# Kernel tuning notes

Measured on AMD Instinct MI355X. Metric: run time of the kernel, lower is better.

The kernel has to match this reference:

```python
import jax, jax.numpy as jnp
import numpy as np

H = 1024
V = 5000
NUM_LAYERS = 2
B, T, U = 2, 128, 64


def setup_inputs() -> dict:
    key = jax.random.key(0)
    ks = jax.random.split(key, 16)
    s = 0.02
    inp = {
        "encoder_out": jax.random.normal(ks[0], (B, T, H), dtype=jnp.float32),
        "targets": jax.random.randint(ks[1], (B, U), 0, V),
        "embed": jax.random.normal(ks[2], (V, H), dtype=jnp.float32) * s,
        # stacked 2-layer LSTM params, PyTorch gate order (i, f, g, o)
        "lstm_Wih": jax.random.normal(ks[3], (NUM_LAYERS, 4 * H, H), dtype=jnp.float32) * s,
        "lstm_Whh": jax.random.normal(ks[4], (NUM_LAYERS, 4 * H, H), dtype=jnp.float32) * s,
        "lstm_bih": jnp.zeros((NUM_LAYERS, 4 * H), dtype=jnp.float32),
        "lstm_bhh": jnp.zeros((NUM_LAYERS, 4 * H), dtype=jnp.float32),
        "enc_W": jax.random.normal(ks[5], (H, H), dtype=jnp.float32) * s,
        "enc_b": jnp.zeros((H,), dtype=jnp.float32),
        "pred_W": jax.random.normal(ks[6], (H, H), dtype=jnp.float32) * s,
        "pred_b": jnp.zeros((H,), dtype=jnp.float32),
        "out_W": jax.random.normal(ks[7], (V + 1, H), dtype=jnp.float32) * s,
        "out_b": jnp.zeros((V + 1,), dtype=jnp.float32),
    }
    return inp


def _lstm_layer(x, Wih, Whh, bih, bhh):
    # x: [B, U, H] -> [B, U, H]; single LSTM layer, PyTorch gate order i,f,g,o
    b, u, h = x.shape
    bias = bih + bhh  # [4H]
    # precompute input projections for all timesteps: [U, B, 4H]
    xg = jnp.einsum('buh,gh->ubg', x, Wih) + bias

    def step(carry, xt):
        hprev, cprev = carry
        gates = xt + hprev @ Whh.T  # [B, 4H]
        i, f, g, o = jnp.split(gates, 4, axis=-1)
        i = jax.nn.sigmoid(i)
        f = jax.nn.sigmoid(f)
        g = jnp.tanh(g)
        o = jax.nn.sigmoid(o)
        c = f * cprev + i * g
        hnew = o * jnp.tanh(c)
        return (hnew, c), hnew

    init = (jnp.zeros((b, h), x.dtype), jnp.zeros((b, h), x.dtype))
    _, hs = jax.lax.scan(step, init, xg)  # hs: [U, B, H]
    return hs.transpose(1, 0, 2)


def reference(encoder_out, targets, embed, lstm_Wih, lstm_Whh, lstm_bih, lstm_bhh,
              enc_W, enc_b, pred_W, pred_b, out_W, out_b):
    # Prediction network: embedding + 2-layer LSTM (deterministic -> no dropout)
    x = embed[targets]  # [B, U, H]
    for l in range(NUM_LAYERS):
        x = _lstm_layer(x, lstm_Wih[l], lstm_Whh[l], lstm_bih[l], lstm_bhh[l])
    pred_out = x  # [B, U, H]

    # Joint network: proj + broadcast add over (T, U) + ReLU + output linear
    enc_p = jnp.einsum('bth,oh->bto', encoder_out, enc_W) + enc_b  # [B, T, H]
    prd_p = jnp.einsum('buh,oh->buo', pred_out, pred_W) + pred_b    # [B, U, H]
    joint = jax.nn.relu(enc_p[:, :, None, :] + prd_p[:, None, :, :])  # [B, T, U, H]
    logits = jnp.einsum('btuh,vh->btuv', joint, out_W) + out_b  # [B, T, U, V+1]
    return logits
```

## Files before the change

kernel.cpp:

```cpp
#include <hip/hip_runtime.h>
#include <hip/hip_bf16.h>

#define B_ 2
#define T_ 128
#define U_ 64
#define H_ 1024
#define NO_ 5001

typedef __attribute__((ext_vector_type(8))) short bf16x8;
typedef __attribute__((ext_vector_type(4))) float f32x4;
typedef __attribute__((ext_vector_type(4))) unsigned int uint4v;

__device__ __forceinline__ float bf2f(unsigned short s) {
  unsigned int u = ((unsigned int)s) << 16;
  float f; __builtin_memcpy(&f, &u, 4); return f;
}
__device__ __forceinline__ unsigned short f2bf(float f) {
  unsigned int u; __builtin_memcpy(&u, &f, 4);
  u = u + 0x7FFFu + ((u >> 16) & 1u);
  return (unsigned short)(u >> 16);
}

__device__ __forceinline__ void gload_lds16(const unsigned short* g, unsigned short* l) {
  __builtin_amdgcn_global_load_lds(
      (const __attribute__((address_space(1))) unsigned int*)g,
      (__attribute__((address_space(3))) unsigned int*)l,
      16, 0, 0);
}

#define R_OUTW 1280256
#define R_WIH  (R_OUTW + 2097152)
#define R_WHH  (R_WIH + 2097152)
#define R_ENCW (R_WHH + 262144)
#define R_PRDW (R_ENCW + 262144)
#define R_ENC  (R_PRDW + 65536)
#define R_BIAS (R_ENC + 1280)

__global__ void k_cvt_all(
    const float* __restrict__ outW, const float* __restrict__ Wih,
    const float* __restrict__ Whh,  const float* __restrict__ encW,
    const float* __restrict__ prdW, const float* __restrict__ enc,
    const float* __restrict__ outB,
    unsigned short* __restrict__ outW_bf, unsigned short* __restrict__ Wih_bf,
    unsigned short* __restrict__ Whh_bf,  unsigned short* __restrict__ encW_bf,
    unsigned short* __restrict__ prdW_bf, unsigned short* __restrict__ enc_bf,
    float* __restrict__ biasPad)
{
  int i = blockIdx.x * 256 + threadIdx.x;
  const float* src; unsigned short* dst; int off;
  if (i < R_OUTW)      { src = outW; dst = outW_bf; off = i; }
  else if (i < R_WIH)  { src = Wih;  dst = Wih_bf;  off = i - R_OUTW; }
  else if (i < R_WHH)  { src = Whh;  dst = Whh_bf;  off = i - R_WIH; }
  else if (i < R_ENCW) { src = encW; dst = encW_bf; off = i - R_WHH; }
  else if (i < R_PRDW) { src = prdW; dst = prdW_bf; off = i - R_ENCW; }
  else if (i < R_ENC)  { src = enc;  dst = enc_bf;  off = i - R_PRDW; }
  else {
    int e0 = (i - R_ENC) * 4;
    float4 v;
    v.x = (e0 + 0 < NO_) ? outB[e0 + 0] : 0.f;
    v.y = (e0 + 1 < NO_) ? outB[e0 + 1] : 0.f;
    v.z = (e0 + 2 < NO_) ? outB[e0 + 2] : 0.f;
    v.w = (e0 + 3 < NO_) ? outB[e0 + 3] : 0.f;
    *(float4*)&biasPad[e0] = v;
    return;
  }
  const float4 v = ((const float4*)src)[off];
  ushort4 o;
  o.x = f2bf(v.x); o.y = f2bf(v.y); o.z = f2bf(v.z); o.w = f2bf(v.w);
  ((ushort4*)dst)[off] = o;
}

__global__ void k_embed(const int* __restrict__ tg, const float* __restrict__ em,
                        unsigned short* __restrict__ x0) {
  int idx = blockIdx.x * 256 + threadIdx.x;
  int bu = idx >> 8;
  int kc = (idx & 255) << 2;
  int t = tg[bu];
  const float4 v = *(const float4*)&em[(long)t * H_ + kc];
  ushort4 o; o.x = f2bf(v.x); o.y = f2bf(v.y); o.z = f2bf(v.z); o.w = f2bf(v.w);
  *(ushort4*)&x0[bu * H_ + kc] = o;
}

__global__ __launch_bounds__(256) void gemm_bt(
    const unsigned short* __restrict__ A, const unsigned short* __restrict__ W,
    const float* __restrict__ b1, const float* __restrict__ b2,
    float* __restrict__ C, int M, int N, int K)
{
  __shared__ unsigned short As[128 * 32];
  __shared__ unsigned short Bs[128 * 32];
  const int tid = threadIdx.x;
  const int n0 = blockIdx.x * 128, m0 = blockIdx.y * 128;
  const int lane = tid & 63, w = tid >> 6;
  const int wr = (w >> 1) * 64, wc = (w & 1) * 64;
  const int lr = lane & 15, lk = (lane >> 4) * 8;
  f32x4 acc[4][4] = {};

  for (int k0 = 0; k0 < K; k0 += 32) {
#pragma unroll
    for (int s = 0; s < 2; ++s) {
      int idx = (w * 2 + s) * 64 + lane;
      int row = idx >> 2, c8 = (idx & 3) * 8;
      gload_lds16(&A[(long)(m0 + row) * K + k0 + c8], &As[(w * 2 + s) * 512]);
      gload_lds16(&W[(long)(n0 + row) * K + k0 + c8], &Bs[(w * 2 + s) * 512]);
    }
    __syncthreads();
    bf16x8 aF[4], bF[4];
#pragma unroll
    for (int i = 0; i < 4; ++i) {
      aF[i] = *(const bf16x8*)&As[(wr + i * 16 + lr) * 32 + lk];
      bF[i] = *(const bf16x8*)&Bs[(wc + i * 16 + lr) * 32 + lk];
    }
#pragma unroll
    for (int i = 0; i < 4; ++i)
#pragma unroll
      for (int j = 0; j < 4; ++j)
        acc[i][j] = __builtin_amdgcn_mfma_f32_16x16x32_bf16(aF[i], bF[j], acc[i][j], 0, 0, 0);
    __syncthreads();
  }

  const int lq = (lane >> 4) * 4;
#pragma unroll
  for (int j = 0; j < 4; ++j) {
    int col = n0 + wc + j * 16 + lr;
    if (col >= N) continue;
    float bb = 0.f;
    if (b1) bb += b1[col];
    if (b2) bb += b2[col];
#pragma unroll
    for (int i = 0; i < 4; ++i) {
      int rowg = m0 + wr + i * 16 + lq;
#pragma unroll
      for (int r = 0; r < 4; ++r)
        C[(long)(rowg + r) * N + col] = acc[i][j][r] + bb;
    }
  }
}

#define STAGE_A(kt2, kh, rb) \
  gload_lds16(aSrc[rb] + (kt2) * 64 + (kh) * 32, \
              &As_f[((((kt2) & 1) * 2 + (kh)) * 8192) + ((rb) * 128 + wv * 16) * 32])
#define STAGE_B(kt2, kh, rb) \
  gload_lds16(bSrc[rb] + (kt2) * 64 + (kh) * 32, \
              &Bs_f[((((kt2) & 1) * 2 + (kh)) * 8192) + ((rb) * 128 + wv * 16) * 32])

__global__ __launch_bounds__(512, 1) void gemm_logits(
    const unsigned short* __restrict__ A, const unsigned short* __restrict__ W,
    const float* __restrict__ biasPad, float* __restrict__ C, int M, int N, int K)
{
  __shared__ __align__(16) unsigned short lds_all[65536];
  unsigned short* As_f = lds_all;
  unsigned short* Bs_f = lds_all + 32768;
  const int tid = threadIdx.x;
  const int lane = tid & 63, wv = tid >> 6;
  const int wm = wv >> 2, wn = wv & 3;
  int swzb = (blockIdx.x & 7) * 160 + (blockIdx.x >> 3);
  const int n0 = (swzb >> 6) * 256;
  const int m0 = (swzb & 63) * 256;
  const int NT = K / 64;

  const unsigned short* aSrc[2];
  const unsigned short* bSrc[2];
#pragma unroll
  for (int rb = 0; rb < 2; ++rb) {
    int rl = rb * 128 + (tid >> 2);
    int c2s = (tid & 3) ^ ((rl >> 1) & 3);
    aSrc[rb] = A + (long)(m0 + rl) * K + c2s * 8;
    bSrc[rb] = W + (long)(n0 + rl) * K + c2s * 8;
  }
  int aOff[8], bOff[4];
#pragma unroll
  for (int i = 0; i < 8; ++i) {
    int r = wm * 128 + i * 16 + (lane & 15);
    aOff[i] = r * 32 + (((lane >> 4) ^ ((r >> 1) & 3)) * 8);
  }
#pragma unroll
  for (int j = 0; j < 4; ++j) {
    int r = wn * 64 + j * 16 + (lane & 15);
    bOff[j] = r * 32 + (((lane >> 4) ^ ((r >> 1) & 3)) * 8);
  }

  f32x4 acc[8][4] = {};

  STAGE_A(0, 0, 0); STAGE_A(0, 0, 1); STAGE_B(0, 0, 0); STAGE_B(0, 0, 1);
  STAGE_A(0, 1, 0); STAGE_A(0, 1, 1); STAGE_B(0, 1, 0); STAGE_B(0, 1, 1);

  for (int kt = 0; kt < NT; ++kt) {
    const int b = kt & 1;
    asm volatile("s_waitcnt vmcnt(4)" ::: "memory");
    __builtin_amdgcn_s_barrier();
    __builtin_amdgcn_sched_barrier(0);
    {
      const int base = (b * 2 + 0) * 8192;
      bf16x8 aF[8], bF[4];
#pragma unroll
      for (int i = 0; i < 8; ++i) aF[i] = *(const bf16x8*)&As_f[base + aOff[i]];
#pragma unroll
      for (int j = 0; j < 4; ++j) bF[j] = *(const bf16x8*)&Bs_f[base + bOff[j]];
      if (kt + 1 < NT) {
        STAGE_A(kt + 1, 0, 0); STAGE_A(kt + 1, 0, 1);
        STAGE_B(kt + 1, 0, 0); STAGE_B(kt + 1, 0, 1);
        STAGE_A(kt + 1, 1, 0); STAGE_A(kt + 1, 1, 1);
      }
      __builtin_amdgcn_s_setprio(1);
#pragma unroll
      for (int i = 0; i < 8; ++i)
#pragma unroll
        for (int j = 0; j < 4; ++j)
          acc[i][j] = __builtin_amdgcn_mfma_f32_16x16x32_bf16(aF[i], bF[j], acc[i][j], 0, 0, 0);
      __builtin_amdgcn_s_setprio(0);
    }
    if (kt + 1 < NT) { asm volatile("s_waitcnt vmcnt(6)" ::: "memory"); }
    else             { asm volatile("s_waitcnt vmcnt(0)" ::: "memory"); }
    __builtin_amdgcn_s_barrier();
    __builtin_amdgcn_sched_barrier(0);
    {
      const int base = (b * 2 + 1) * 8192;
      bf16x8 aF[8], bF[4];
#pragma unroll
      for (int i = 0; i < 8; ++i) aF[i] = *(const bf16x8*)&As_f[base + aOff[i]];
#pragma unroll
      for (int j = 0; j < 4; ++j) bF[j] = *(const bf16x8*)&Bs_f[base + bOff[j]];
      if (kt + 1 < NT) { STAGE_B(kt + 1, 1, 0); STAGE_B(kt + 1, 1, 1); }
      __builtin_amdgcn_s_setprio(1);
#pragma unroll
      for (int i = 0; i < 8; ++i)
#pragma unroll
        for (int j = 0; j < 4; ++j)
          acc[i][j] = __builtin_amdgcn_mfma_f32_16x16x32_bf16(aF[i], bF[j], acc[i][j], 0, 0, 0);
      __builtin_amdgcn_s_setprio(0);
    }
  }

  float* eb = (float*)lds_all;
  const int lq = (lane >> 4) * 4;
  float bv4[4];
#pragma unroll
  for (int j = 0; j < 4; ++j) bv4[j] = biasPad[n0 + wn * 64 + j * 16 + (lane & 15)];

#pragma unroll
  for (int cp = 0; cp < 4; ++cp) {
    __syncthreads();
#pragma unroll
    for (int ii = 0; ii < 2; ++ii) {
      int rbase = wm * 32 + ii * 16 + lq;
#pragma unroll
      for (int j = 0; j < 4; ++j) {
        int col = wn * 64 + j * 16 + (lane & 15);
#pragma unroll
        for (int r = 0; r < 4; ++r)
          eb[(rbase + r) * 261 + col] = acc[cp * 2 + ii][j][r] + bv4[j];
      }
    }
    __syncthreads();
    {
      int rl = tid >> 3, ci = tid & 7;
      long grow = (long)m0 + (rl >> 5) * 128 + cp * 32 + (rl & 31);
      float* crow = C + grow * N + n0;
      const float* er = &eb[rl * 261];
#pragma unroll
      for (int k = 0; k < 8; ++k) {
        int col = ci * 4 + k * 32;
        float4 v = *(const float4*)&er[col];
        int gc = n0 + col;
        if (gc + 4 <= N) {
          *(float4*)&crow[col] = v;
        } else if (gc < N) {
          float tmp[4] = {v.x, v.y, v.z, v.w};
#pragma unroll
          for (int e = 0; e < 4; ++e)
            if (gc + e < N) crow[col + e] = tmp[e];
        }
      }
    }
  }
}

__global__ __launch_bounds__(256, 1) void lstm_fused3(
    const float* __restrict__ xg0,
    const unsigned short* __restrict__ Whh0,
    const unsigned short* __restrict__ Whh1,
    const unsigned short* __restrict__ Wih1,
    const float* __restrict__ bih1, const float* __restrict__ bhh1,
    unsigned short* __restrict__ x2_bf,
    float* __restrict__ hbuf0,
    float* __restrict__ hbuf1,
    float* __restrict__ xbuf,
    float* __restrict__ xgbuf,
    int*   __restrict__ flagsx)
{
  __shared__ float hs[2][H_];
  __shared__ float xgs[128][64];
  __shared__ float part[4][64][2];
  __shared__ float gv[2][64];
  __shared__ float bias2s[64];

  const int tid = threadIdx.x;
  const int grp = blockIdx.x >> 6;
  const int bid = blockIdx.x & 63;
  const int w = tid >> 6, l = tid & 63;
  const int g = l >> 4, q = l & 15;
  const int row = g * 1024 + bid * 16 + q;
  const int kb = w * 256;

  if (grp == 0) {
    bf16x8 wreg[32];
#pragma unroll
    for (int it = 0; it < 32; ++it)
      wreg[it] = *(const bf16x8*)&Whh0[(long)row * H_ + kb + it * 8];
#pragma unroll
    for (int rep = 0; rep < 8; ++rep) {
      int c = rep * 256 + tid;
      int r2 = c >> 4, sub = c & 15;
      int gg = sub >> 2, f4 = sub & 3;
      const float4 v = *(const float4*)&xg0[(long)r2 * 4096 + gg * 1024 + bid * 16 + f4 * 4];
      *(float4*)&xgs[r2][gg * 16 + f4 * 4] = v;
    }
    __syncthreads();

    float creg = 0.f;
    for (int u = 0; u < U_; ++u) {
      float a00 = 0.f, a01 = 0.f, a02 = 0.f, a03 = 0.f;
      float a10 = 0.f, a11 = 0.f, a12 = 0.f, a13 = 0.f;
      if (u > 0) {
        const float thr = 4.0f * u - 2.0f;
        const float* base = hbuf0 + (u & 1) * 2 * H_;
        const float* pa = base + tid * 4;
        const float* pb = base + H_ + tid * 4;
        float4 va, vb;
        for (;;) {
          asm volatile("global_load_dwordx4 %0, %2, off sc1\n\t"
                       "global_load_dwordx4 %1, %3, off sc1\n\t"
                       "s_waitcnt vmcnt(0)"
                       : "=v"(va), "=v"(vb) : "v"(pa), "v"(pb) : "memory");
          if (va.x > thr && va.y > thr && va.z > thr && va.w > thr &&
              vb.x > thr && vb.y > thr && vb.z > thr && vb.w > thr) break;
        }
        const float off = 4.0f * u;
        va.x -= off; va.y -= off; va.z -= off; va.w -= off;
        vb.x -= off; vb.y -= off; vb.z -= off; vb.w -= off;
        *(float4*)&hs[0][tid * 4] = va;
        *(float4*)&hs[1][tid * 4] = vb;
        __syncthreads();
#pragma unroll
        for (int it = 0; it < 32; ++it) {
          bf16x8 wv = wreg[it];
          float4 h0a = *(const float4*)&hs[0][kb + it * 8];
          float4 h0b = *(const float4*)&hs[0][kb + it * 8 + 4];
          float4 h1a = *(const float4*)&hs[1][kb + it * 8];
          float4 h1b = *(const float4*)&hs[1][kb + it * 8 + 4];
          a00 += bf2f((unsigned short)wv[0]) * h0a.x + bf2f((unsigned short)wv[4]) * h0b.x;
          a01 += bf2f((unsigned short)wv[1]) * h0a.y + bf2f((unsigned short)wv[5]) * h0b.y;
          a02 += bf2f((unsigned short)wv[2]) * h0a.z + bf2f((unsigned short)wv[6]) * h0b.z;
          a03 += bf2f((unsigned short)wv[3]) * h0a.w + bf2f((unsigned short)wv[7]) * h0b.w;
          a10 += bf2f((unsigned short)wv[0]) * h1a.x + bf2f((unsigned short)wv[4]) * h1b.x;
          a11 += bf2f((unsigned short)wv[1]) * h1a.y + bf2f((unsigned short)wv[5]) * h1b.y;
          a12 += bf2f((unsigned short)wv[2]) * h1a.z + bf2f((unsigned short)wv[6]) * h1b.z;
          a13 += bf2f((unsigned short)wv[3]) * h1a.w + bf2f((unsigned short)wv[7]) * h1b.w;
        }
      }
      part[w][l][0] = (a00 + a01) + (a02 + a03);
      part[w][l][1] = (a10 + a11) + (a12 + a13);
      __syncthreads();
      if (tid < 128) {
        int b = tid >> 6, ll = tid & 63;
        gv[b][ll] = part[0][ll][b] + part[1][ll][b] + part[2][ll][b] + part[3][ll][b]
                  + xgs[b * 64 + u][ll];
      }
      __syncthreads();
      if (tid < 32) {
        int b = tid >> 4, qq = tid & 15;
        float gi = gv[b][qq], gf = gv[b][16 + qq], gc = gv[b][32 + qq], go = gv[b][48 + qq];
        float i_ = 1.f / (1.f + expf(-gi));
        float f_ = 1.f / (1.f + expf(-gf));
        float g_ = tanhf(gc);
        float o_ = 1.f / (1.f + expf(-go));
        creg = f_ * creg + i_ * g_;
        float h = o_ * tanhf(creg);
        int j = bid * 16 + qq;
        float tvx = h + 4.0f;
        const float* px = &xbuf[u * 2 * H_ + b * H_ + j];
        asm volatile("global_store_dword %0, %1, off sc1" :: "v"(px), "v"(tvx) : "memory");
        if (u < U_ - 1) {
          float tv = h + 4.0f * (u + 1);
          const float* p = &hbuf0[((u + 1) & 1) * 2 * H_ + b * H_ + j];
          asm volatile("global_store_dword %0, %1, off sc1" :: "v"(p), "v"(tv) : "memory");
        }
      }
    }
  } else if (grp == 1) {
    bf16x8 wreg[32];
#pragma unroll
    for (int it = 0; it < 32; ++it)
      wreg[it] = *(const bf16x8*)&Wih1[(long)row * H_ + kb + it * 8];
    if (tid < 64) {
      int rr = (tid >> 4) * 1024 + bid * 16 + (tid & 15);
      bias2s[tid] = bih1[rr] + bhh1[rr];
    }
    __syncthreads();

    for (int u = 0; u < U_; ++u) {
      const float* base = xbuf + u * 2 * H_;
      const float* pa = base + tid * 4;
      const float* pb = base + H_ + tid * 4;
      float4 va, vb;
      for (;;) {
        asm volatile("global_load_dwordx4 %0, %2, off sc1\n\t"
                     "global_load_dwordx4 %1, %3, off sc1\n\t"
                     "s_waitcnt vmcnt(0)"
                     : "=v"(va), "=v"(vb) : "v"(pa), "v"(pb) : "memory");
        if (va.x > 2.f && va.y > 2.f && va.z > 2.f && va.w > 2.f &&
            vb.x > 2.f && vb.y > 2.f && vb.z > 2.f && vb.w > 2.f) break;
        __builtin_amdgcn_s_sleep(2);
      }
      va.x -= 4.f; va.y -= 4.f; va.z -= 4.f; va.w -= 4.f;
      vb.x -= 4.f; vb.y -= 4.f; vb.z -= 4.f; vb.w -= 4.f;
      *(float4*)&hs[0][tid * 4] = va;
      *(float4*)&hs[1][tid * 4] = vb;
      __syncthreads();

      float a00 = 0.f, a01 = 0.f, a02 = 0.f, a03 = 0.f;
      float a10 = 0.f, a11 = 0.f, a12 = 0.f, a13 = 0.f;
#pragma unroll
      for (int it = 0; it < 32; ++it) {
        bf16x8 wv = wreg[it];
        float4 h0a = *(const float4*)&hs[0][kb + it * 8];
        float4 h0b = *(const float4*)&hs[0][kb + it * 8 + 4];
        float4 h1a = *(const float4*)&hs[1][kb + it * 8];
        float4 h1b = *(const float4*)&hs[1][kb + it * 8 + 4];
        a00 += bf2f((unsigned short)wv[0]) * h0a.x + bf2f((unsigned short)wv[4]) * h0b.x;
        a01 += bf2f((unsigned short)wv[1]) * h0a.y + bf2f((unsigned short)wv[5]) * h0b.y;
        a02 += bf2f((unsigned short)wv[2]) * h0a.z + bf2f((unsigned short)wv[6]) * h0b.z;
        a03 += bf2f((unsigned short)wv[3]) * h0a.w + bf2f((unsigned short)wv[7]) * h0b.w;
        a10 += bf2f((unsigned short)wv[0]) * h1a.x + bf2f((unsigned short)wv[4]) * h1b.x;
        a11 += bf2f((unsigned short)wv[1]) * h1a.y + bf2f((unsigned short)wv[5]) * h1b.y;
        a12 += bf2f((unsigned short)wv[2]) * h1a.z + bf2f((unsigned short)wv[6]) * h1b.z;
        a13 += bf2f((unsigned short)wv[3]) * h1a.w + bf2f((unsigned short)wv[7]) * h1b.w;
      }
      part[w][l][0] = (a00 + a01) + (a02 + a03);
      part[w][l][1] = (a10 + a11) + (a12 + a13);
      __syncthreads();
      if (tid < 128) {
        int b = tid >> 6, ll = tid & 63;
        float s = part[0][ll][b] + part[1][ll][b] + part[2][ll][b] + part[3][ll][b]
                + bias2s[ll];
        const float* p = &xgbuf[((u * 64 + bid) * 2 + b) * 64 + ll];
        asm volatile("global_store_dword %0, %1, off sc1" :: "v"(p), "v"(s) : "memory");
        asm volatile("s_waitcnt vmcnt(0)" ::: "memory");
      }
      __syncthreads();
      if (tid == 0) {
        int one = 1;
        const int* fp = &flagsx[(u * 64 + bid) * 16];
        asm volatile("global_store_dword %0, %1, off sc1" :: "v"(fp), "v"(one) : "memory");
      }
    }
  } else {
    bf16x8 wreg[32];
#pragma unroll
    for (int it = 0; it < 32; ++it)
      wreg[it] = *(const bf16x8*)&Whh1[(long)row * H_ + kb + it * 8];
    __syncthreads();

    float creg = 0.f;
    for (int u = 0; u < U_; ++u) {
      {
        const int* fp = &flagsx[(u * 64 + bid) * 16];
        int fv;
        do {
          asm volatile("global_load_dword %0, %1, off sc1\n\ts_waitcnt vmcnt(0)"
                       : "=v"(fv) : "v"(fp) : "memory");
        } while (fv == 0);
      }
      float xgv = 0.f;
      if (tid < 128) {
        const float* p = &xgbuf[((u * 64 + bid) * 2 + (tid >> 6)) * 64 + (tid & 63)];
        asm volatile("global_load_dword %0, %1, off sc1\n\ts_waitcnt vmcnt(0)"
                     : "=v"(xgv) : "v"(p) : "memory");
      }
      float a00 = 0.f, a01 = 0.f, a02 = 0.f, a03 = 0.f;
      float a10 = 0.f, a11 = 0.f, a12 = 0.f, a13 = 0.f;
      if (u > 0) {
        const float thr = 4.0f * u - 2.0f;
        const float* base = hbuf1 + (u & 1) * 2 * H_;
        const float* pa = base + tid * 4;
        const float* pb = base + H_ + tid * 4;
        float4 va, vb;
        for (;;) {
          asm volatile("global_load_dwordx4 %0, %2, off sc1\n\t"
                       "global_load_dwordx4 %1, %3, off sc1\n\t"
                       "s_waitcnt vmcnt(0)"
                       : "=v"(va), "=v"(vb) : "v"(pa), "v"(pb) : "memory");
          if (va.x > thr && va.y > thr && va.z > thr && va.w > thr &&
              vb.x > thr && vb.y > thr && vb.z > thr && vb.w > thr) break;
        }
        const float off = 4.0f * u;
        va.x -= off; va.y -= off; va.z -= off; va.w -= off;
        vb.x -= off; vb.y -= off; vb.z -= off; vb.w -= off;
        *(float4*)&hs[0][tid * 4] = va;
        *(float4*)&hs[1][tid * 4] = vb;
        __syncthreads();
#pragma unroll
        for (int it = 0; it < 32; ++it) {
          bf16x8 wv = wreg[it];
          float4 h0a = *(const float4*)&hs[0][kb + it * 8];
          float4 h0b = *(const float4*)&hs[0][kb + it * 8 + 4];
          float4 h1a = *(const float4*)&hs[1][kb + it * 8];
          float4 h1b = *(const float4*)&hs[1][kb + it * 8 + 4];
          a00 += bf2f((unsigned short)wv[0]) * h0a.x + bf2f((unsigned short)wv[4]) * h0b.x;
          a01 += bf2f((unsigned short)wv[1]) * h0a.y + bf2f((unsigned short)wv[5]) * h0b.y;
          a02 += bf2f((unsigned short)wv[2]) * h0a.z + bf2f((unsigned short)wv[6]) * h0b.z;
          a03 += bf2f((unsigned short)wv[3]) * h0a.w + bf2f((unsigned short)wv[7]) * h0b.w;
          a10 += bf2f((unsigned short)wv[0]) * h1a.x + bf2f((unsigned short)wv[4]) * h1b.x;
          a11 += bf2f((unsigned short)wv[1]) * h1a.y + bf2f((unsigned short)wv[5]) * h1b.y;
          a12 += bf2f((unsigned short)wv[2]) * h1a.z + bf2f((unsigned short)wv[6]) * h1b.z;
          a13 += bf2f((unsigned short)wv[3]) * h1a.w + bf2f((unsigned short)wv[7]) * h1b.w;
        }
      }
      part[w][l][0] = (a00 + a01) + (a02 + a03);
      part[w][l][1] = (a10 + a11) + (a12 + a13);
      __syncthreads();
      if (tid < 128) {
        int b = tid >> 6, ll = tid & 63;
        gv[b][ll] = part[0][ll][b] + part[1][ll][b] + part[2][ll][b] + part[3][ll][b]
                  + xgv;
      }
      __syncthreads();
      if (tid < 32) {
        int b = tid >> 4, qq = tid & 15;
        float gi = gv[b][qq], gf = gv[b][16 + qq], gc = gv[b][32 + qq], go = gv[b][48 + qq];
        float i_ = 1.f / (1.f + expf(-gi));
        float f_ = 1.f / (1.f + expf(-gf));
        float g_ = tanhf(gc);
        float o_ = 1.f / (1.f + expf(-go));
        creg = f_ * creg + i_ * g_;
        float h = o_ * tanhf(creg);
        int j = bid * 16 + qq;
        x2_bf[(b * U_ + u) * H_ + j] = f2bf(h);
        if (u < U_ - 1) {
          float tv = h + 4.0f * (u + 1);
          const float* p = &hbuf1[((u + 1) & 1) * 2 * H_ + b * H_ + j];
          asm volatile("global_store_dword %0, %1, off sc1" :: "v"(p), "v"(tv) : "memory");
        }
      }
    }
  }
}

__global__ void k_joint(const float* __restrict__ ep, const float* __restrict__ pp,
                        unsigned short* __restrict__ jt)
{
  int idx = blockIdx.x * 256 + threadIdx.x;
  int m = idx >> 8;
  int kc = (idx & 255) << 2;
  int erow = m >> 6;
  int prow = (m >> 13) * U_ + (m & 63);
  const float4 e = *(const float4*)&ep[erow * H_ + kc];
  const float4 p = *(const float4*)&pp[prow * H_ + kc];
  float4 s;
  s.x = fmaxf(e.x + p.x, 0.f); s.y = fmaxf(e.y + p.y, 0.f);
  s.z = fmaxf(e.z + p.z, 0.f); s.w = fmaxf(e.w + p.w, 0.f);
  ushort4 o; o.x = f2bf(s.x); o.y = f2bf(s.y); o.z = f2bf(s.z); o.w = f2bf(s.w);
  *(ushort4*)&jt[m * H_ + kc] = o;
}

extern "C" void kernel_launch(void* const* d_in, const int* in_sizes, int n_in,
                              void* d_out, int out_size, void* d_ws, size_t ws_size,
                              hipStream_t stream)
{
  const float* enc   = (const float*)d_in[0];
  const int*   tg    = (const int*)d_in[1];
  const float* em    = (const float*)d_in[2];
  const float* Wih   = (const float*)d_in[3];
  const float* Whh   = (const float*)d_in[4];
  const float* bih   = (const float*)d_in[5];
  const float* bhh   = (const float*)d_in[6];
  const float* encW  = (const float*)d_in[7];
  const float* encB  = (const float*)d_in[8];
  const float* prdW  = (const float*)d_in[9];
  const float* prdB  = (const float*)d_in[10];
  const float* outW  = (const float*)d_in[11];
  const float* outB  = (const float*)d_in[12];
  float* out = (float*)d_out;
  char* ws = (char*)d_ws;

  unsigned short* outW_bf = (unsigned short*)(ws + 0);
  unsigned short* Wih_bf  = (unsigned short*)(ws + 10485760);
  unsigned short* Whh_bf  = (unsigned short*)(ws + 27262976);
  unsigned short* encW_bf = (unsigned short*)(ws + 44040192);
  unsigned short* prdW_bf = (unsigned short*)(ws + 46137344);
  unsigned short* enc_bf  = (unsigned short*)(ws + 48234496);
  unsigned short* x0_bf   = (unsigned short*)(ws + 48758784);
  unsigned short* x2_bf   = (unsigned short*)(ws + 49283072);
  float* xg  = (float*)(ws + 49545216);
  float* hbufL0 = (float*)(ws + 51642368);
  unsigned short* jt = (unsigned short*)(ws + 51659008);
  float* hbufL1 = (float*)(ws + 85213440);
  float* biasPad = (float*)(ws + 85229824);
  float* xbuf = (float*)(ws + 85250304);
  int* flagsx = (int*)(ws + 85774592);
  float* xgbuf = xg;
  float* ep = xg;
  float* pp = (float*)(ws + 49545216 + 1048576);

  hipMemsetAsync(hbufL0, 0, 16384, stream);
  hipMemsetAsync(hbufL1, 0, 16384, stream);
  hipMemsetAsync(xbuf, 0, 524288, stream);
  hipMemsetAsync(flagsx, 0, 262144, stream);

  k_cvt_all<<<R_BIAS / 256, 256, 0, stream>>>(
      outW, Wih, Whh, encW, prdW, enc, outB,
      outW_bf, Wih_bf, Whh_bf, encW_bf, prdW_bf, enc_bf, biasPad);
  k_embed<<<(B_ * U_ * H_ / 4) / 256, 256, 0, stream>>>(tg, em, x0_bf);

  gemm_bt<<<dim3(32, 1), 256, 0, stream>>>(x0_bf, Wih_bf, bih, bhh, xg, B_ * U_, 4096, H_);
  lstm_fused3<<<192, 256, 0, stream>>>(xg, Whh_bf, Whh_bf + 4096 * H_, Wih_bf + 4096 * H_,
                                       bih + 4096, bhh + 4096, x2_bf,
                                       hbufL0, hbufL1, xbuf, xgbuf, flagsx);

  gemm_bt<<<dim3(8, 2), 256, 0, stream>>>(enc_bf, encW_bf, encB, nullptr, ep, B_ * T_, H_, H_);
  gemm_bt<<<dim3(8, 1), 256, 0, stream>>>(x2_bf, prdW_bf, prdB, nullptr, pp, B_ * U_, H_, H_);

  k_joint<<<16384, 256, 0, stream>>>(ep, pp, jt);
  gemm_logits<<<1280, 512, 0, stream>>>(jt, outW_bf, biasPad, out, B_ * T_ * U_, NO_, H_);
}
```

Measured before the change: 663.2 us.

## Cut LSTM step barriers, use fast gate math, merge projection GEMMs and memsets

In the fused LSTM kernel the partial sums are double-buffered by step parity. This drops one __syncthreads per step and the gv reduction stage, since the 32 gate threads now reduce the partials themselves. Sigmoid and tanh switch to clamped __expf/rcp versions. The encoder and prediction projection GEMMs are merged into one launch, and three memsets become one contiguous memset. The aim is to shorten the serial per-step latency of the recurrence and cut launch overhead. The cost is slightly less accurate activations and a removed barrier between the LDS hs write and the dot product, which looks like a possible race.

```diff
diff --git a/kernel.cpp b/kernel.cpp
--- a/kernel.cpp
+++ b/kernel.cpp
@@ -19,6 +19,16 @@
   unsigned int u; __builtin_memcpy(&u, &f, 4);
   u = u + 0x7FFFu + ((u >> 16) & 1u);
   return (unsigned short)(u >> 16);
+}
+__device__ __forceinline__ float fsig(float x) {
+  x = fminf(fmaxf(x, -30.f), 30.f);
+  float e = __expf(-x);
+  return __builtin_amdgcn_rcpf(1.f + e);
+}
+__device__ __forceinline__ float ftanh(float x) {
+  x = fminf(fmaxf(x, -15.f), 15.f);
+  float e = __expf(2.f * x);
+  return (e - 1.f) * __builtin_amdgcn_rcpf(e + 1.f);
 }
 
 __device__ __forceinline__ void gload_lds16(const unsigned short* g, unsigned short* l) {
@@ -136,6 +146,64 @@
   }
 }
 
+__global__ __launch_bounds__(256) void gemm_proj(
+    const unsigned short* __restrict__ enc_bf, const unsigned short* __restrict__ x2_bf,
+    const unsigned short* __restrict__ encW_bf, const unsigned short* __restrict__ prdW_bf,
+    const float* __restrict__ encB, const float* __restrict__ prdB,
+    float* __restrict__ ep, float* __restrict__ pp)
+{
+  __shared__ unsigned short As[128 * 32];
+  __shared__ unsigned short Bs[128 * 32];
+  const int tid = threadIdx.x;
+  const unsigned short* A; const unsigned short* W; const float* b1; float* C;
+  int m0;
+  if (blockIdx.y < 2) { A = enc_bf; W = encW_bf; b1 = encB; C = ep; m0 = blockIdx.y * 128; }
+  else                { A = x2_bf;  W = prdW_bf; b1 = prdB; C = pp; m0 = 0; }
+  const int n0 = blockIdx.x * 128;
+  const int K = H_, N = H_;
+  const int lane = tid & 63, w = tid >> 6;
+  const int wr = (w >> 1) * 64, wc = (w & 1) * 64;
+  const int lr = lane & 15, lk = (lane >> 4) * 8;
+  f32x4 acc[4][4] = {};
+
+  for (int k0 = 0; k0 < K; k0 += 32) {
+#pragma unroll
+    for (int s = 0; s < 2; ++s) {
+      int idx = (w * 2 + s) * 64 + lane;
+      int row = idx >> 2, c8 = (idx & 3) * 8;
+      gload_lds16(&A[(long)(m0 + row) * K + k0 + c8], &As[(w * 2 + s) * 512]);
+      gload_lds16(&W[(long)(n0 + row) * K + k0 + c8], &Bs[(w * 2 + s) * 512]);
+    }
+    __syncthreads();
+    bf16x8 aF[4], bF[4];
+#pragma unroll
+    for (int i = 0; i < 4; ++i) {
+      aF[i] = *(const bf16x8*)&As[(wr + i * 16 + lr) * 32 + lk];
+      bF[i] = *(const bf16x8*)&Bs[(wc + i * 16 + lr) * 32 + lk];
+    }
+#pragma unroll
+    for (int i = 0; i < 4; ++i)
+#pragma unroll
+      for (int j = 0; j < 4; ++j)
+        acc[i][j] = __builtin_amdgcn_mfma_f32_16x16x32_bf16(aF[i], bF[j], acc[i][j], 0, 0, 0);
+    __syncthreads();
+  }
+
+  const int lq = (lane >> 4) * 4;
+#pragma unroll
+  for (int j = 0; j < 4; ++j) {
+    int col = n0 + wc + j * 16 + lr;
+    float bb = b1[col];
+#pragma unroll
+    for (int i = 0; i < 4; ++i) {
+      int rowg = m0 + wr + i * 16 + lq;
+#pragma unroll
+      for (int r = 0; r < 4; ++r)
+        C[(long)(rowg + r) * N + col] = acc[i][j][r] + bb;
+    }
+  }
+}
+
 #define STAGE_A(kt2, kh, rb) \
   gload_lds16(aSrc[rb] + (kt2) * 64 + (kh) * 32, \
               &As_f[((((kt2) & 1) * 2 + (kh)) * 8192) + ((rb) * 128 + wv * 16) * 32])
@@ -290,8 +358,7 @@
 {
   __shared__ float hs[2][H_];
   __shared__ float xgs[128][64];
-  __shared__ float part[4][64][2];
-  __shared__ float gv[2][64];
+  __shared__ float part[2][4][64][2];
   __shared__ float bias2s[64];
 
   const int tid = threadIdx.x;
@@ -302,6 +369,24 @@
   const int row = g * 1024 + bid * 16 + q;
   const int kb = w * 256;
 
+#define DOT_BODY(WREG, SRC)                                                              \
+  _Pragma("unroll")                                                                      \
+  for (int it = 0; it < 32; ++it) {                                                      \
+    bf16x8 wv = WREG[it];                                                                \
+    float4 h0a = *(const float4*)&SRC[0][kb + it * 8];                                   \
+    float4 h0b = *(const float4*)&SRC[0][kb + it * 8 + 4];                               \
+    float4 h1a = *(const float4*)&SRC[1][kb + it * 8];                                   \
+    float4 h1b = *(const float4*)&SRC[1][kb + it * 8 + 4];                               \
+    a00 += bf2f((unsigned short)wv[0]) * h0a.x + bf2f((unsigned short)wv[4]) * h0b.x;    \
+    a01 += bf2f((unsigned short)wv[1]) * h0a.y + bf2f((unsigned short)wv[5]) * h0b.y;    \
+    a02 += bf2f((unsigned short)wv[2]) * h0a.z + bf2f((unsigned short)wv[6]) * h0b.z;    \
+    a03 += bf2f((unsigned short)wv[3]) * h0a.w + bf2f((unsigned short)wv[7]) * h0b.w;    \
+    a10 += bf2f((unsigned short)wv[0]) * h1a.x + bf2f((unsigned short)wv[4]) * h1b.x;    \
+    a11 += bf2f((unsigned short)wv[1]) * h1a.y + bf2f((unsigned short)wv[5]) * h1b.y;    \
+    a12 += bf2f((unsigned short)wv[2]) * h1a.z + bf2f((unsigned short)wv[6]) * h1b.z;    \
+    a13 += bf2f((unsigned short)wv[3]) * h1a.w + bf2f((unsigned short)wv[7]) * h1b.w;    \
+  }
+
   if (grp == 0) {
     bf16x8 wreg[32];
 #pragma unroll
@@ -319,6 +404,7 @@
 
     float creg = 0.f;
     for (int u = 0; u < U_; ++u) {
+      const int p = u & 1;
       float a00 = 0.f, a01 = 0.f, a02 = 0.f, a03 = 0.f;
       float a10 = 0.f, a11 = 0.f, a12 = 0.f, a13 = 0.f;
       if (u > 0) {
@@ -340,50 +426,33 @@
         vb.x -= off; vb.y -= off; vb.z -= off; vb.w -= off;
         *(float4*)&hs[0][tid * 4] = va;
         *(float4*)&hs[1][tid * 4] = vb;
-        __syncthreads();
-#pragma unroll
-        for (int it = 0; it < 32; ++it) {
-          bf16x8 wv = wreg[it];
-          float4 h0a = *(const float4*)&hs[0][kb + it * 8];
-          float4 h0b = *(const float4*)&hs[0][kb + it * 8 + 4];
-          float4 h1a = *(const float4*)&hs[1][kb + it * 8];
-          float4 h1b = *(const float4*)&hs[1][kb + it * 8 + 4];
-          a00 += bf2f((unsigned short)wv[0]) * h0a.x + bf2f((unsigned short)wv[4]) * h0b.x;
-          a01 += bf2f((unsigned short)wv[1]) * h0a.y + bf2f((unsigned short)wv[5]) * h0b.y;
-          a02 += bf2f((unsigned short)wv[2]) * h0a.z + bf2f((unsigned short)wv[6]) * h0b.z;
-          a03 += bf2f((unsigned short)wv[3]) * h0a.w + bf2f((unsigned short)wv[7]) * h0b.w;
-          a10 += bf2f((unsigned short)wv[0]) * h1a.x + bf2f((unsigned short)wv[4]) * h1b.x;
-          a11 += bf2f((unsigned short)wv[1]) * h1a.y + bf2f((unsigned short)wv[5]) * h1b.y;
-          a12 += bf2f((unsigned short)wv[2]) * h1a.z + bf2f((unsigned short)wv[6]) * h1b.z;
-          a13 += bf2f((unsigned short)wv[3]) * h1a.w + bf2f((unsigned short)wv[7]) * h1b.w;
-        }
-      }
-      part[w][l][0] = (a00 + a01) + (a02 + a03);
-      part[w][l][1] = (a10 + a11) + (a12 + a13);
-      __syncthreads();
-      if (tid < 128) {
-        int b = tid >> 6, ll = tid & 63;
-        gv[b][ll] = part[0][ll][b] + part[1][ll][b] + part[2][ll][b] + part[3][ll][b]
-                  + xgs[b * 64 + u][ll];
-      }
+        DOT_BODY(wreg, hs)
+      }
+      part[p][w][l][0] = (a00 + a01) + (a02 + a03);
+      part[p][w][l][1] = (a10 + a11) + (a12 + a13);
       __syncthreads();
       if (tid < 32) {
         int b = tid >> 4, qq = tid & 15;
-        float gi = gv[b][qq], gf = gv[b][16 + qq], gc = gv[b][32 + qq], go = gv[b][48 + qq];
-        float i_ = 1.f / (1.f + expf(-gi));
-        float f_ = 1.f / (1.f + expf(-gf));
-        float g_ = tanhf(gc);
-        float o_ = 1.f / (1.f + expf(-go));
+        int bu = b * 64 + u;
+        float gi = part[p][0][qq][b] + part[p][1][qq][b] + part[p][2][qq][b]
+                 + part[p][3][qq][b] + xgs[bu][qq];
+        float gf = part[p][0][16 + qq][b] + part[p][1][16 + qq][b] + part[p][2][16 + qq][b]
+                 + part[p][3][16 + qq][b] + xgs[bu][16 + qq];
+        float gc = part[p][0][32 + qq][b] + part[p][1][32 + qq][b] + part[p][2][32 + qq][b]
+                 + part[p][3][32 + qq][b] + xgs[bu][32 + qq];
+        float go = part[p][0][48 + qq][b] + part[p][1][48 + qq][b] + part[p][2][48 + qq][b]
+                 + part[p][3][48 + qq][b] + xgs[bu][48 + qq];
+        float i_ = fsig(gi), f_ = fsig(gf), g_ = ftanh(gc), o_ = fsig(go);
         creg = f_ * creg + i_ * g_;
-        float h = o_ * tanhf(creg);
+        float h = o_ * ftanh(creg);
         int j = bid * 16 + qq;
         float tvx = h + 4.0f;
         const float* px = &xbuf[u * 2 * H_ + b * H_ + j];
         asm volatile("global_store_dword %0, %1, off sc1" :: "v"(px), "v"(tvx) : "memory");
         if (u < U_ - 1) {
           float tv = h + 4.0f * (u + 1);
-          const float* p = &hbuf0[((u + 1) & 1) * 2 * H_ + b * H_ + j];
-          asm volatile("global_store_dword %0, %1, off sc1" :: "v"(p), "v"(tv) : "memory");
+          const float* pp2 = &hbuf0[((u + 1) & 1) * 2 * H_ + b * H_ + j];
+          asm volatile("global_store_dword %0, %1, off sc1" :: "v"(pp2), "v"(tv) : "memory");
         }
       }
     }
@@ -399,6 +468,7 @@
     __syncthreads();
 
     for (int u = 0; u < U_; ++u) {
+      const int p = u & 1;
       const float* base = xbuf + u * 2 * H_;
       const float* pa = base + tid * 4;
       const float* pb = base + H_ + tid * 4;
@@ -416,35 +486,19 @@
       vb.x -= 4.f; vb.y -= 4.f; vb.z -= 4.f; vb.w -= 4.f;
       *(float4*)&hs[0][tid * 4] = va;
       *(float4*)&hs[1][tid * 4] = vb;
-      __syncthreads();
 
       float a00 = 0.f, a01 = 0.f, a02 = 0.f, a03 = 0.f;
       float a10 = 0.f, a11 = 0.f, a12 = 0.f, a13 = 0.f;
-#pragma unroll
-      for (int it = 0; it < 32; ++it) {
-        bf16x8 wv = wreg[it];
-        float4 h0a = *(const float4*)&hs[0][kb + it * 8];
-        float4 h0b = *(const float4*)&hs[0][kb + it * 8 + 4];
-        float4 h1a = *(const float4*)&hs[1][kb + it * 8];
-        float4 h1b = *(const float4*)&hs[1][kb + it * 8 + 4];
-        a00 += bf2f((unsigned short)wv[0]) * h0a.x + bf2f((unsigned short)wv[4]) * h0b.x;
-        a01 += bf2f((unsigned short)wv[1]) * h0a.y + bf2f((unsigned short)wv[5]) * h0b.y;
-        a02 += bf2f((unsigned short)wv[2]) * h0a.z + bf2f((unsigned short)wv[6]) * h0b.z;
-        a03 += bf2f((unsigned short)wv[3]) * h0a.w + bf2f((unsigned short)wv[7]) * h0b.w;
-        a10 += bf2f((unsigned short)wv[0]) * h1a.x + bf2f((unsigned short)wv[4]) * h1b.x;
-        a11 += bf2f((unsigned short)wv[1]) * h1a.y + bf2f((unsigned short)wv[5]) * h1b.y;
-        a12 += bf2f((unsigned short)wv[2]) * h1a.z + bf2f((unsigned short)wv[6]) * h1b.z;
-        a13 += bf2f((unsigned short)wv[3]) * h1a.w + bf2f((unsigned short)wv[7]) * h1b.w;
-      }
-      part[w][l][0] = (a00 + a01) + (a02 + a03);
-      part[w][l][1] = (a10 + a11) + (a12 + a13);
+      DOT_BODY(wreg, hs)
+      part[p][w][l][0] = (a00 + a01) + (a02 + a03);
+      part[p][w][l][1] = (a10 + a11) + (a12 + a13);
       __syncthreads();
       if (tid < 128) {
         int b = tid >> 6, ll = tid & 63;
-        float s = part[0][ll][b] + part[1][ll][b] + part[2][ll][b] + part[3][ll][b]
-                + bias2s[ll];
-        const float* p = &xgbuf[((u * 64 + bid) * 2 + b) * 64 + ll];
-        asm volatile("global_store_dword %0, %1, off sc1" :: "v"(p), "v"(s) : "memory");
+        float s = part[p][0][ll][b] + part[p][1][ll][b] + part[p][2][ll][b]
+                + part[p][3][ll][b] + bias2s[ll];
+        const float* pw = &xgbuf[((u * 64 + bid) * 2 + b) * 64 + ll];
+        asm volatile("global_store_dword %0, %1, off sc1" :: "v"(pw), "v"(s) : "memory");
         asm volatile("s_waitcnt vmcnt(0)" ::: "memory");
       }
       __syncthreads();
@@ -463,6 +517,7 @@
 
     float creg = 0.f;
     for (int u = 0; u < U_; ++u) {
+      const int p = u & 1;
       {
         const int* fp = &flagsx[(u * 64 + bid) * 16];
         int fv;
@@ -471,11 +526,15 @@
                        : "=v"(fv) : "v"(fp) : "memory");
         } while (fv == 0);
       }
-      float xgv = 0.f;
-      if (tid < 128) {
-        const float* p = &xgbuf[((u * 64 + bid) * 2 + (tid >> 6)) * 64 + (tid & 63)];
-        asm volatile("global_load_dword %0, %1, off sc1\n\ts_waitcnt vmcnt(0)"
-                     : "=v"(xgv) : "v"(p) : "memory");
+      float xgi = 0.f, xgf = 0.f, xgg = 0.f, xgo = 0.f;
+      if (tid < 32) {
+        int b = tid >> 4, qq = tid & 15;
+        const float* xb = &xgbuf[((u * 64 + bid) * 2 + b) * 64];
+        asm volatile("global_load_dword %0, %1, off sc1" : "=v"(xgi) : "v"(xb + qq) : "memory");
+        asm volatile("global_load_dword %0, %1, off sc1" : "=v"(xgf) : "v"(xb + 16 + qq) : "memory");
+        asm volatile("global_load_dword %0, %1, off sc1" : "=v"(xgg) : "v"(xb + 32 + qq) : "memory");
+        asm volatile("global_load_dword %0, %1, off sc1" : "=v"(xgo) : "v"(xb + 48 + qq) : "memory");
+        asm volatile("s_waitcnt vmcnt(0)" ::: "memory");
       }
       float a00 = 0.f, a01 = 0.f, a02 = 0.f, a03 = 0.f;
       float a10 = 0.f, a11 = 0.f, a12 = 0.f, a13 = 0.f;
@@ -498,52 +557,35 @@
         vb.x -= off; vb.y -= off; vb.z -= off; vb.w -= off;
         *(float4*)&hs[0][tid * 4] = va;
         *(float4*)&hs[1][tid * 4] = vb;
-        __syncthreads();
-#pragma unroll
-        for (int it = 0; it < 32; ++it) {
-          bf16x8 wv = wreg[it];
-          float4 h0a = *(const float4*)&hs[0][kb + it * 8];
-          float4 h0b = *(const float4*)&hs[0][kb + it * 8 + 4];
-          float4 h1a = *(const float4*)&hs[1][kb + it * 8];
-          float4 h1b = *(const float4*)&hs[1][kb + it * 8 + 4];
-          a00 += bf2f((unsigned short)wv[0]) * h0a.x + bf2f((unsigned short)wv[4]) * h0b.x;
-          a01 += bf2f((unsigned short)wv[1]) * h0a.y + bf2f((unsigned short)wv[5]) * h0b.y;
-          a02 += bf2f((unsigned short)wv[2]) * h0a.z + bf2f((unsigned short)wv[6]) * h0b.z;
-          a03 += bf2f((unsigned short)wv[3]) * h0a.w + bf2f((unsigned short)wv[7]) * h0b.w;
-          a10 += bf2f((unsigned short)wv[0]) * h1a.x + bf2f((unsigned short)wv[4]) * h1b.x;
-          a11 += bf2f((unsigned short)wv[1]) * h1a.y + bf2f((unsigned short)wv[5]) * h1b.y;
-          a12 += bf2f((unsigned short)wv[2]) * h1a.z + bf2f((unsigned short)wv[6]) * h1b.z;
-          a13 += bf2f((unsigned short)wv[3]) * h1a.w + bf2f((unsigned short)wv[7]) * h1b.w;
-        }
-      }
-      part[w][l][0] = (a00 + a01) + (a02 + a03);
-      part[w][l][1] = (a10 + a11) + (a12 + a13);
-      __syncthreads();
-      if (tid < 128) {
-        int b = tid >> 6, ll = tid & 63;
-        gv[b][ll] = part[0][ll][b] + part[1][ll][b] + part[2][ll][b] + part[3][ll][b]
-                  + xgv;
-      }
+        DOT_BODY(wreg, hs)
+      }
+      part[p][w][l][0] = (a00 + a01) + (a02 + a03);
+      part[p][w][l][1] = (a10 + a11) + (a12 + a13);
       __syncthreads();
       if (tid < 32) {
         int b = tid >> 4, qq = tid & 15;
-        float gi = gv[b][qq], gf = gv[b][16 + qq], gc = gv[b][32 + qq], go = gv[b][48 + qq];
-        float i_ = 1.f / (1.f + expf(-gi));
-        float f_ = 1.f / (1.f + expf(-gf));
-        float g_ = tanhf(gc);
-        float o_ = 1.f / (1.f + expf(-go));
+        float gi = part[p][0][qq][b] + part[p][1][qq][b] + part[p][2][qq][b]
+                 + part[p][3][qq][b] + xgi;
+        float gf = part[p][0][16 + qq][b] + part[p][1][16 + qq][b] + part[p][2][16 + qq][b]
+                 + part[p][3][16 + qq][b] + xgf;
+        float gc = part[p][0][32 + qq][b] + part[p][1][32 + qq][b] + part[p][2][32 + qq][b]
+                 + part[p][3][32 + qq][b] + xgg;
+        float go = part[p][0][48 + qq][b] + part[p][1][48 + qq][b] + part[p][2][48 + qq][b]
+                 + part[p][3][48 + qq][b] + xgo;
+        float i_ = fsig(gi), f_ = fsig(gf), g_ = ftanh(gc), o_ = fsig(go);
         creg = f_ * creg + i_ * g_;
-        float h = o_ * tanhf(creg);
+        float h = o_ * ftanh(creg);
         int j = bid * 16 + qq;
         x2_bf[(b * U_ + u) * H_ + j] = f2bf(h);
         if (u < U_ - 1) {
           float tv = h + 4.0f * (u + 1);
-          const float* p = &hbuf1[((u + 1) & 1) * 2 * H_ + b * H_ + j];
-          asm volatile("global_store_dword %0, %1, off sc1" :: "v"(p), "v"(tv) : "memory");
+          const float* pp2 = &hbuf1[((u + 1) & 1) * 2 * H_ + b * H_ + j];
+          asm volatile("global_store_dword %0, %1, off sc1" :: "v"(pp2), "v"(tv) : "memory");
         }
       }
     }
   }
+#undef DOT_BODY
 }
 
 __global__ void k_joint(const float* __restrict__ ep, const float* __restrict__ pp,
@@ -603,9 +645,7 @@
   float* pp = (float*)(ws + 49545216 + 1048576);
 
   hipMemsetAsync(hbufL0, 0, 16384, stream);
-  hipMemsetAsync(hbufL1, 0, 16384, stream);
-  hipMemsetAsync(xbuf, 0, 524288, stream);
-  hipMemsetAsync(flagsx, 0, 262144, stream);
+  hipMemsetAsync(hbufL1, 0, 86036736 - 85213440, stream);
 
   k_cvt_all<<<R_BIAS / 256, 256, 0, stream>>>(
       outW, Wih, Whh, encW, prdW, enc, outB,
@@ -617,8 +657,8 @@
                                        bih + 4096, bhh + 4096, x2_bf,
                                        hbufL0, hbufL1, xbuf, xgbuf, flagsx);
 
-  gemm_bt<<<dim3(8, 2), 256, 0, stream>>>(enc_bf, encW_bf, encB, nullptr, ep, B_ * T_, H_, H_);
-  gemm_bt<<<dim3(8, 1), 256, 0, stream>>>(x2_bf, prdW_bf, prdB, nullptr, pp, B_ * U_, H_, H_);
+  gemm_proj<<<dim3(8, 3), 256, 0, stream>>>(enc_bf, x2_bf, encW_bf, prdW_bf,
+                                            encB, prdB, ep, pp);
 
   k_joint<<<16384, 256, 0, stream>>>(ep, pp, jt);
   gemm_logits<<<1280, 512, 0, stream>>>(jt, outW_bf, biasPad, out, B_ * T_ * U_, NO_, H_);
```

Result: faster. 611.6 us (-7.8%).
